# Kernel optimization log

Measured on AMD Instinct MI355X. Metric: run time of the kernel, lower is better.

The kernel has to match this reference:

```python
import jax, jax.numpy as jnp
import numpy as np

D = 128          # latent_dim
N = 40000        # num nodes
B = 8            # num graphs in batch
S = N // B       # nodes per graph
K = 6            # knn
E = 640000       # spatial edges
FF = 256         # ffn hidden


def glorot(key, shape):
    lim = jnp.sqrt(6.0 / (shape[0] + shape[-1]))
    return jax.random.uniform(key, shape, minval=-lim, maxval=lim, dtype=jnp.float32)


def setup_inputs() -> dict:
    key = jax.random.key(0)
    ks = jax.random.split(key, 24)
    inp = {
        "x": jax.random.normal(ks[0], (N, D), dtype=jnp.float32),
        "edge_index": jax.random.randint(ks[1], (2, E), 0, N, dtype=jnp.int64),
        "edge_attr": jax.random.uniform(ks[2], (E, 1), dtype=jnp.float32),
        "batch": jnp.repeat(jnp.arange(B, dtype=jnp.int64), S),
        # spatial GATv2Conv params
        "W_sl": glorot(ks[3], (D, D)), "b_sl": jnp.zeros((D,), jnp.float32),
        "W_sr": glorot(ks[4], (D, D)), "b_sr": jnp.zeros((D,), jnp.float32),
        "att_s": glorot(ks[5], (D,)), "W_se": glorot(ks[6], (1, D)),
        "bias_s": jnp.zeros((D,), jnp.float32),
        # latent GATv2Conv params (no edge features)
        "W_ll": glorot(ks[7], (D, D)), "b_ll": jnp.zeros((D,), jnp.float32),
        "W_lr": glorot(ks[8], (D, D)), "b_lr": jnp.zeros((D,), jnp.float32),
        "att_l": glorot(ks[9], (D,)), "bias_l": jnp.zeros((D,), jnp.float32),
        # concat_skip fusion linear: in = 2*D
        "W_c": glorot(ks[10], (2 * D, D)), "b_c": jnp.zeros((D,), jnp.float32),
        # FFN
        "W_f1": glorot(ks[11], (D, FF)), "b_f1": jnp.zeros((FF,), jnp.float32),
        "W_f2": glorot(ks[12], (FF, D)), "b_f2": jnp.zeros((D,), jnp.float32),
    }
    return inp


def relu6(v):
    return jnp.clip(v, 0.0, 6.0)


def segment_softmax(logits, seg, num_segments):
    m = jax.ops.segment_max(logits, seg, num_segments=num_segments)
    e = jnp.exp(logits - m[seg])
    s = jax.ops.segment_sum(e, seg, num_segments=num_segments)
    return e / s[seg]


def gatv2(x, src, dst, edge_feat, W_l, b_l, W_r, b_r, att, bias):
    """PyG GATv2Conv, heads=1, concat=True, negative_slope=0.2."""
    xl = x @ W_l + b_l            # [N,D] source transform
    xr = x @ W_r + b_r            # [N,D] target transform
    h = xl[src] + xr[dst]         # [E,D]
    if edge_feat is not None:
        h = h + edge_feat         # [E,D] already projected by lin_edge
    h = jax.nn.leaky_relu(h, 0.2)
    alpha = h @ att               # [E]
    alpha = segment_softmax(alpha, dst, N)
    out = jax.ops.segment_sum(xl[src] * alpha[:, None], dst, num_segments=N)
    return out + bias


def knn_edges(x):
    """knn_graph(k=K, loop=False, flow='source_to_target') per graph, plus
    the self loops that latent GATv2Conv adds (add_self_loops=True)."""
    xs = jax.lax.stop_gradient(x).reshape(B, S, D)
    sq = jnp.sum(xs * xs, axis=-1)                       # [B,S]
    d2 = sq[:, :, None] + sq[:, None, :] - 2.0 * jnp.einsum('bid,bjd->bij', xs, xs)
    d2 = jnp.where(jnp.eye(S, dtype=bool)[None], jnp.inf, d2)
    _, idx = jax.lax.top_k(-d2, K)                       # [B,S,K] neighbor ids
    offs = (jnp.arange(B) * S)[:, None, None]
    src = (idx + offs).reshape(-1)                       # neighbors -> sources
    dst = jnp.repeat(jnp.arange(N), K)                   # query nodes -> targets
    loop = jnp.arange(N)
    return jnp.concatenate([src, loop]), jnp.concatenate([dst, loop])


def reference(x, edge_index, edge_attr, batch,
              W_sl, b_sl, W_sr, b_sr, att_s, W_se, bias_s,
              W_ll, b_ll, W_lr, b_lr, att_l, bias_l,
              W_c, b_c, W_f1, b_f1, W_f2, b_f2):
    # spatial channel: GATv2 with scalar edge attr
    e_feat = edge_attr @ W_se                            # lin_edge, [E,D]
    ch_sp = gatv2(x, edge_index[0], edge_index[1], e_feat,
                  W_sl, b_sl, W_sr, b_sr, att_s, bias_s)
    # latent channel: dynamic kNN graph + GATv2
    src_l, dst_l = knn_edges(x)
    ch_lat = gatv2(x, src_l, dst_l, None,
                   W_ll, b_ll, W_lr, b_lr, att_l, bias_l)
    # fusion = concat_skip
    fused = jnp.concatenate([ch_sp, ch_lat], axis=-1) @ W_c + b_c + x
    # FFN block (norms are Identity), residual
    ffn = relu6(fused @ W_f1 + b_f1) @ W_f2 + b_f2
    out = fused + ffn
    # plain_last=False -> final activation relu6
    return relu6(out)
```

## Files before the change

### kernel.cpp

```cpp
#include <hip/hip_runtime.h>
#include <math.h>

constexpr int N  = 40000;
constexpr int D  = 128;
constexpr int E  = 640000;
constexpr int Bg = 8;
constexpr int Sg = 5000;
constexpr int KN = 6;
constexpr int FF = 256;
constexpr int QLEN = 1280;
constexpr int NCAND = 48;

typedef short short8 __attribute__((ext_vector_type(8)));
typedef float f32x4  __attribute__((ext_vector_type(4)));

__device__ __forceinline__ unsigned short f2bf(float f)
{
    unsigned int u = __float_as_uint(f);
    return (unsigned short)((u + 0x7fffu + ((u >> 16) & 1u)) >> 16);
}

__device__ __forceinline__ unsigned umin2(unsigned a, unsigned b) { return a < b ? a : b; }

__global__ __launch_bounds__(256) void w_prep_k(
    const float* __restrict__ W0, const float* __restrict__ W1,
    const float* __restrict__ W2, const float* __restrict__ W3,
    const float* __restrict__ Wc, const float* __restrict__ Wf1,
    const float* __restrict__ Wf2,
    unsigned short* __restrict__ wt4, unsigned short* __restrict__ wtc,
    unsigned short* __restrict__ wtf1, unsigned short* __restrict__ wtf2)
{
    int idx = blockIdx.x * 256 + threadIdx.x;
    if (idx < 65536) {
        int m = idx >> 14, rem = idx & 16383;
        int k = rem & 127, c = rem >> 7;
        const float* Wm = (m == 0) ? W0 : (m == 1) ? W1 : (m == 2) ? W2 : W3;
        wt4[m * 16384 + c * 128 + k] = f2bf(Wm[k * 128 + c]);
    } else if (idx < 98304) {
        int rem = idx - 65536; int k = rem & 255, c = rem >> 8;
        wtc[c * 256 + k] = f2bf(Wc[k * 128 + c]);
    } else if (idx < 131072) {
        int rem = idx - 98304; int k = rem & 127, c = rem >> 7;
        wtf1[c * 128 + k] = f2bf(Wf1[k * 256 + c]);
    } else {
        int rem = idx - 131072; int k = rem & 255, c = rem >> 8;
        wtf2[c * 256 + k] = f2bf(Wf2[k * 128 + c]);
    }
}

__global__ __launch_bounds__(256) void gemm_mfma_k(
    const float* __restrict__ A, int lda,
    const unsigned short* __restrict__ Wt, int Kdim,
    const float* __restrict__ bias,
    const float* __restrict__ res,
    float* __restrict__ out, int ldo, int act)
{
    __shared__ float xs[64][36];
    __shared__ unsigned short ws[128][40];
    int tid = threadIdx.x;
    int w = tid >> 6, lane = tid & 63;
    int lg = lane >> 4, ln = lane & 15;
    int r0 = blockIdx.x * 64;
    int cb = blockIdx.y * 128;

    f32x4 acc[8];
#pragma unroll
    for (int ct = 0; ct < 8; ++ct) acc[ct] = {0.f, 0.f, 0.f, 0.f};

    int srow = tid >> 2, sk8 = (tid & 3) * 8;
    int wcol = tid >> 1, wk = (tid & 1) * 16;

    for (int kt = 0; kt < Kdim; kt += 32) {
        __syncthreads();
        *(float4*)&xs[srow][sk8]     = *(const float4*)&A[(size_t)(r0 + srow) * lda + kt + sk8];
        *(float4*)&xs[srow][sk8 + 4] = *(const float4*)&A[(size_t)(r0 + srow) * lda + kt + sk8 + 4];
        *(short8*)&ws[wcol][wk]     = *(const short8*)&Wt[(size_t)(cb + wcol) * Kdim + kt + wk];
        *(short8*)&ws[wcol][wk + 8] = *(const short8*)&Wt[(size_t)(cb + wcol) * Kdim + kt + wk + 8];
        __syncthreads();

        int arow = w * 16 + ln;
        f32x4 a0 = *(const f32x4*)&xs[arow][lg * 8];
        f32x4 a1 = *(const f32x4*)&xs[arow][lg * 8 + 4];
        float af[8] = {a0[0], a0[1], a0[2], a0[3], a1[0], a1[1], a1[2], a1[3]};
        short8 ah, al;
#pragma unroll
        for (int i = 0; i < 8; ++i) {
            unsigned short h = f2bf(af[i]);
            ah[i] = (short)h;
            float hf = __uint_as_float(((unsigned)h) << 16);
            al[i] = (short)f2bf(af[i] - hf);
        }
#pragma unroll
        for (int ct = 0; ct < 8; ++ct) {
            short8 bw = *(const short8*)&ws[ct * 16 + ln][lg * 8];
            acc[ct] = __builtin_amdgcn_mfma_f32_16x16x32_bf16(ah, bw, acc[ct], 0, 0, 0);
            acc[ct] = __builtin_amdgcn_mfma_f32_16x16x32_bf16(al, bw, acc[ct], 0, 0, 0);
        }
    }

#pragma unroll
    for (int ct = 0; ct < 8; ++ct) {
        int c = cb + ct * 16 + ln;
        float bv = bias[c];
#pragma unroll
        for (int rg = 0; rg < 4; ++rg) {
            int r = r0 + w * 16 + lg * 4 + rg;
            float v = acc[ct][rg] + bv;
            if (res) v += res[(size_t)r * 128 + c];
            if (act) v = fminf(fmaxf(v, 0.f), 6.f);
            out[(size_t)r * ldo + c] = v;
        }
    }
}

__global__ __launch_bounds__(256) void gemm4_mfma_k(
    const float* __restrict__ A, const unsigned short* __restrict__ wt4,
    const float* __restrict__ b0, const float* __restrict__ b1,
    const float* __restrict__ b2, const float* __restrict__ b3,
    float* __restrict__ o0, float* __restrict__ o1,
    float* __restrict__ o2, float* __restrict__ o3)
{
    const unsigned short* Wt = wt4 + blockIdx.y * 16384;
    const float* bias; float* out;
    if (blockIdx.y == 0)      { bias = b0; out = o0; }
    else if (blockIdx.y == 1) { bias = b1; out = o1; }
    else if (blockIdx.y == 2) { bias = b2; out = o2; }
    else                      { bias = b3; out = o3; }

    __shared__ float xs[64][36];
    __shared__ unsigned short ws[128][40];
    int tid = threadIdx.x;
    int w = tid >> 6, lane = tid & 63;
    int lg = lane >> 4, ln = lane & 15;
    int r0 = blockIdx.x * 64;

    f32x4 acc[8];
#pragma unroll
    for (int ct = 0; ct < 8; ++ct) acc[ct] = {0.f, 0.f, 0.f, 0.f};

    int srow = tid >> 2, sk8 = (tid & 3) * 8;
    int wcol = tid >> 1, wk = (tid & 1) * 16;

    for (int kt = 0; kt < 128; kt += 32) {
        __syncthreads();
        *(float4*)&xs[srow][sk8]     = *(const float4*)&A[(size_t)(r0 + srow) * 128 + kt + sk8];
        *(float4*)&xs[srow][sk8 + 4] = *(const float4*)&A[(size_t)(r0 + srow) * 128 + kt + sk8 + 4];
        *(short8*)&ws[wcol][wk]     = *(const short8*)&Wt[(size_t)wcol * 128 + kt + wk];
        *(short8*)&ws[wcol][wk + 8] = *(const short8*)&Wt[(size_t)wcol * 128 + kt + wk + 8];
        __syncthreads();

        int arow = w * 16 + ln;
        f32x4 a0 = *(const f32x4*)&xs[arow][lg * 8];
        f32x4 a1 = *(const f32x4*)&xs[arow][lg * 8 + 4];
        float af[8] = {a0[0], a0[1], a0[2], a0[3], a1[0], a1[1], a1[2], a1[3]};
        short8 ah, al;
#pragma unroll
        for (int i = 0; i < 8; ++i) {
            unsigned short h = f2bf(af[i]);
            ah[i] = (short)h;
            float hf = __uint_as_float(((unsigned)h) << 16);
            al[i] = (short)f2bf(af[i] - hf);
        }
#pragma unroll
        for (int ct = 0; ct < 8; ++ct) {
            short8 bw = *(const short8*)&ws[ct * 16 + ln][lg * 8];
            acc[ct] = __builtin_amdgcn_mfma_f32_16x16x32_bf16(ah, bw, acc[ct], 0, 0, 0);
            acc[ct] = __builtin_amdgcn_mfma_f32_16x16x32_bf16(al, bw, acc[ct], 0, 0, 0);
        }
    }

#pragma unroll
    for (int ct = 0; ct < 8; ++ct) {
        int c = ct * 16 + ln;
        float bv = bias[c];
#pragma unroll
        for (int rg = 0; rg < 4; ++rg) {
            int r = r0 + w * 16 + lg * 4 + rg;
            out[(size_t)r * 128 + c] = acc[ct][rg] + bv;
        }
    }
}

__global__ __launch_bounds__(256) void prep_k(const float* __restrict__ x,
                                              unsigned short* __restrict__ xh,
                                              float* __restrict__ sqn)
{
    int w = threadIdx.x >> 6, lane = threadIdx.x & 63;
    int row = blockIdx.x * 4 + w;
    float2 v = *(const float2*)&x[(size_t)row * 128 + lane * 2];
    ushort2 h = make_ushort2(f2bf(v.x), f2bf(v.y));
    *(ushort2*)&xh[(size_t)row * 128 + lane * 2] = h;
    float s = fmaf(v.y, v.y, v.x * v.x);
#pragma unroll
    for (int off = 32; off; off >>= 1) s += __shfl_xor(s, off);
    if (lane == 0) sqn[row] = s;
}

__device__ __forceinline__ void ins6(unsigned (&d)[6], unsigned k)
{
#pragma unroll
    for (int t = 0; t < 6; ++t) {
        unsigned lo = d[t] < k ? d[t] : k;
        unsigned hi = d[t] < k ? k : d[t];
        d[t] = lo; k = hi;
    }
}

__global__ __launch_bounds__(256) void knn_mfma_k(const unsigned short* __restrict__ xh,
                                                  const float* __restrict__ sqn,
                                                  int* __restrict__ cand)
{
    __shared__ char lds[16640];
    char* ldsH = lds;
    float* cs_s = (float*)(lds + 16384);

    int b = blockIdx.x;
    int g = b & 7, r = b >> 3;
    int qtr = r & 3, qblk = r >> 2;
    int gbase = g * Sg;
    int cbase = qtr * QLEN;
    int qlen = (qtr < 3) ? QLEN : (Sg - 3 * QLEN);
    int ntiles = (qlen + 63) >> 6;
    int nfull = (qtr < 3) ? ntiles : ntiles - 1;
    int tid = threadIdx.x;
    int w = tid >> 6, lane = tid & 63;
    int lg = lane >> 4, ln = lane & 15;
    int q0 = qblk * 128 + w * 32;

    short8 bh[2][4];
#pragma unroll
    for (int s = 0; s < 2; ++s) {
        int q = q0 + s * 16 + ln;
        int qrow = gbase + (q < Sg ? q : Sg - 1);
#pragma unroll
        for (int ks = 0; ks < 4; ++ks)
            bh[s][ks] = *(const short8*)&xh[(size_t)qrow * 128 + ks * 32 + lg * 8];
    }

    int srow = tid >> 4, sslot = tid & 15;
    int sw_st = (srow & 7) << 4;
    int dstoff[4];
    const unsigned short* src[4];
#pragma unroll
    for (int i = 0; i < 4; ++i) {
        int row = i * 16 + srow;
        dstoff[i] = row * 256 + ((sslot * 16) ^ sw_st);
        src[i] = &xh[(size_t)(gbase + cbase + row) * 128 + sslot * 8];
    }
    const float* csrc = &sqn[gbase + cbase];

    unsigned d6a[6], d6b[6];
#pragma unroll
    for (int t = 0; t < 6; ++t) { d6a[t] = 0xFFFFFFFFu; d6b[t] = 0xFFFFFFFFu; }

    for (int t64 = 0; t64 < ntiles; ++t64) {
        __syncthreads();
        if (t64 < nfull) {
#pragma unroll
            for (int i = 0; i < 4; ++i) {
                short8 vh = *(const short8*)src[i];
                src[i] += 64 * 128;
                *(short8*)(ldsH + dstoff[i]) = vh;
            }
            if (tid < 64) cs_s[tid] = csrc[tid] + 1024.0f;
        } else {
            int c0 = cbase + t64 * 64;
#pragma unroll
            for (int i = 0; i < 4; ++i) {
                int cr = c0 + i * 16 + srow;
                if (cr >= Sg) cr = Sg - 1;
                short8 vh = *(const short8*)&xh[(size_t)(gbase + cr) * 128 + sslot * 8];
                *(short8*)(ldsH + dstoff[i]) = vh;
            }
            if (tid < 64) {
                int cl = c0 + tid;
                cs_s[tid] = (cl < cbase + qlen) ? (sqn[gbase + cl] + 1024.0f) : __builtin_inff();
            }
        }
        csrc += 64;
        __syncthreads();

        int c0 = cbase + t64 * 64;
#pragma unroll
        for (int g16 = 0; g16 < 4; ++g16) {
            f32x4 acc0 = {0.f, 0.f, 0.f, 0.f};
            f32x4 acc1 = {0.f, 0.f, 0.f, 0.f};
            int rr = g16 * 16 + ln;
            int rsw = (ln & 7) << 4;
#pragma unroll
            for (int ks = 0; ks < 4; ++ks) {
                short8 ah = *(const short8*)(ldsH + rr * 256 + ((lg * 16 + ks * 64) ^ rsw));
                acc0 = __builtin_amdgcn_mfma_f32_16x16x32_bf16(ah, bh[0][ks], acc0, 0, 0, 0);
                acc1 = __builtin_amdgcn_mfma_f32_16x16x32_bf16(ah, bh[1][ks], acc1, 0, 0, 0);
            }
            f32x4 cv = *(const f32x4*)&cs_s[g16 * 16 + lg * 4];
            int idx0 = (c0 - cbase) + g16 * 16 + lg * 4;
            unsigned kb0[4], kb1[4];
#pragma unroll
            for (int rg = 0; rg < 4; ++rg) {
                kb0[rg] = __float_as_uint(fmaf(-2.f, acc0[rg], cv[rg]));
                kb1[rg] = __float_as_uint(fmaf(-2.f, acc1[rg], cv[rg]));
            }
            unsigned mn0 = umin2(umin2(kb0[0], kb0[1]), umin2(kb0[2], kb0[3]));
            unsigned mn1 = umin2(umin2(kb1[0], kb1[1]), umin2(kb1[2], kb1[3]));
            if ((mn0 & 0xFFFFF800u) < d6a[5]) {
#pragma unroll
                for (int rg = 0; rg < 4; ++rg) {
                    unsigned k = (kb0[rg] & 0xFFFFF800u) | (unsigned)(idx0 + rg);
                    if (k < d6a[5]) ins6(d6a, k);
                }
            }
            if ((mn1 & 0xFFFFF800u) < d6b[5]) {
#pragma unroll
                for (int rg = 0; rg < 4; ++rg) {
                    unsigned k = (kb1[rg] & 0xFFFFF800u) | (unsigned)(idx0 + rg);
                    if (k < d6b[5]) ins6(d6b, k);
                }
            }
        }
    }

#pragma unroll
    for (int s = 0; s < 2; ++s) {
        unsigned m12[12];
#pragma unroll
        for (int t = 0; t < 6; ++t) m12[t] = s ? d6b[t] : d6a[t];
#pragma unroll
        for (int t = 6; t < 12; ++t) m12[t] = 0xFFFFFFFFu;
#pragma unroll
        for (int sg = 1; sg < 4; ++sg)
#pragma unroll
            for (int t = 0; t < 6; ++t) {
                unsigned v = __shfl(s ? d6b[t] : d6a[t], ln + sg * 16);
#pragma unroll
                for (int u = 0; u < 12; ++u) {
                    unsigned lo = m12[u] < v ? m12[u] : v;
                    unsigned hi = m12[u] < v ? v : m12[u];
                    m12[u] = lo; v = hi;
                }
            }
        int q = q0 + s * 16 + ln;
        if (lg == 0 && q < Sg) {
            int* cp = &cand[(size_t)(gbase + q) * NCAND + qtr * 12];
#pragma unroll
            for (int t = 0; t < 12; ++t) cp[t] = gbase + cbase + (int)(m12[t] & 2047u);
        }
    }
}

__global__ __launch_bounds__(256) void knn_rerank_k(const float* __restrict__ x,
                                                    const float* __restrict__ sqn,
                                                    const int* __restrict__ cand,
                                                    int* __restrict__ knn_idx)
{
    int w = threadIdx.x >> 6, lane = threadIdx.x & 63;
    int grp = lane >> 4, gl = lane & 15;
    int q = blockIdx.x * 4 + w;
    float4 qa = *(const float4*)&x[(size_t)q * 128 + gl * 8];
    float4 qb = *(const float4*)&x[(size_t)q * 128 + gl * 8 + 4];
    const int* cp = &cand[(size_t)q * NCAND + grp * 12];

    float d6[6]; int i6[6]; float mx = __builtin_inff(); int sl = 0;
#pragma unroll
    for (int t = 0; t < 6; ++t) { d6[t] = __builtin_inff(); i6[t] = -1; }

#pragma unroll 2
    for (int j = 0; j < 12; ++j) {
        int c = cp[j];
        bool ok = (unsigned)c < (unsigned)N && c != q;
        int ca = ok ? c : 0;
        float4 va = *(const float4*)&x[(size_t)ca * 128 + gl * 8];
        float4 vb = *(const float4*)&x[(size_t)ca * 128 + gl * 8 + 4];
        float p = qa.x * va.x;
        p = fmaf(qa.y, va.y, p); p = fmaf(qa.z, va.z, p); p = fmaf(qa.w, va.w, p);
        p = fmaf(qb.x, vb.x, p); p = fmaf(qb.y, vb.y, p);
        p = fmaf(qb.z, vb.z, p); p = fmaf(qb.w, vb.w, p);
#pragma unroll
        for (int off = 1; off < 16; off <<= 1) p += __shfl_xor(p, off);
        float dv = ok ? fmaf(-2.f, p, sqn[ca]) : __builtin_inff();
        if (dv < mx) {
#pragma unroll
            for (int t = 0; t < 6; ++t)
                if (t == sl) { d6[t] = dv; i6[t] = c; }
            float m2 = d6[0]; int s2 = 0;
#pragma unroll
            for (int t = 1; t < 6; ++t)
                if (d6[t] > m2) { m2 = d6[t]; s2 = t; }
            mx = m2; sl = s2;
        }
    }

#pragma unroll
    for (int sg = 1; sg < 4; ++sg) {
#pragma unroll
        for (int t = 0; t < 6; ++t) {
            float dv = __shfl(d6[t], gl + sg * 16);
            int ci = __shfl(i6[t], gl + sg * 16);
            if (grp == 0 && dv < mx) {
#pragma unroll
                for (int u = 0; u < 6; ++u)
                    if (u == sl) { d6[u] = dv; i6[u] = ci; }
                float m2 = d6[0]; int s2 = 0;
#pragma unroll
                for (int u = 1; u < 6; ++u)
                    if (d6[u] > m2) { m2 = d6[u]; s2 = u; }
                mx = m2; sl = s2;
            }
        }
    }
    if (lane < 6) {
        int v;
#pragma unroll
        for (int t = 0; t < 6; ++t) if (t == lane) v = i6[t];
        knn_idx[(size_t)q * 6 + lane] = v;
    }
}

__global__ __launch_bounds__(256) void hist_k(const int* __restrict__ dstA, int* __restrict__ deg)
{
    int e = blockIdx.x * 256 + threadIdx.x;
    atomicAdd(&deg[dstA[e]], 1);
}

__global__ __launch_bounds__(1024) void scan_k(const int* __restrict__ deg, int* __restrict__ rowptr)
{
    __shared__ int ps[1024];
    int t = threadIdx.x;
    const int chunk = 40;
    int base = t * chunk;
    int s = 0;
    for (int k = 0; k < chunk; ++k) { int i = base + k; if (i < N) s += deg[i]; }
    ps[t] = s;
    __syncthreads();
    for (int off = 1; off < 1024; off <<= 1) {
        int v = (t >= off) ? ps[t - off] : 0;
        __syncthreads();
        ps[t] += v;
        __syncthreads();
    }
    int run = ps[t] - s;
    for (int k = 0; k < chunk; ++k) {
        int i = base + k;
        if (i < N) { rowptr[i] = run; run += deg[i]; }
    }
    if (t == 0) rowptr[N] = E;
}

__global__ __launch_bounds__(256) void scatter_k(const int* __restrict__ srcA, const int* __restrict__ dstA,
                                                 const float* __restrict__ ea,
                                                 const int* __restrict__ rowptr, int* __restrict__ cnt,
                                                 int* __restrict__ csr_src, float* __restrict__ csr_ea)
{
    int e = blockIdx.x * 256 + threadIdx.x;
    int d = dstA[e];
    int pos = rowptr[d] + atomicAdd(&cnt[d], 1);
    csr_src[pos] = srcA[e];
    csr_ea[pos] = ea[e];
}

__global__ __launch_bounds__(256) void gat_fused_k(
    const float* __restrict__ xl_s, const float* __restrict__ xr_s,
    const int* __restrict__ rowptr, const int* __restrict__ csr_src, const float* __restrict__ csr_ea,
    const float* __restrict__ att_s, const float* __restrict__ wse, const float* __restrict__ bias_s,
    const float* __restrict__ xl_l, const float* __restrict__ xr_l,
    const int* __restrict__ knn, const float* __restrict__ att_l, const float* __restrict__ bias_l,
    float* __restrict__ ch2)
{
    int w = threadIdx.x >> 6, lane = threadIdx.x & 63;
    int dst = blockIdx.x * 4 + w;

    if (blockIdx.y == 0) {
        int base = rowptr[dst];
        int deg = rowptr[dst + 1] - base;
        float xr0 = xr_s[(size_t)dst * 128 + lane], xr1 = xr_s[(size_t)dst * 128 + 64 + lane];
        float at0 = att_s[lane], at1 = att_s[64 + lane];
        float we0 = wse[lane], we1 = wse[64 + lane];

        float m = -1e30f, ssum = 0.f, o0 = 0.f, o1 = 0.f;
        for (int i = 0; i < deg; ++i) {
            int s = csr_src[base + i];
            float ea = csr_ea[base + i];
            float v0 = xl_s[(size_t)s * 128 + lane];
            float v1 = xl_s[(size_t)s * 128 + 64 + lane];
            float h0 = fmaf(ea, we0, v0 + xr0);
            float h1 = fmaf(ea, we1, v1 + xr1);
            h0 = h0 > 0.f ? h0 : 0.2f * h0;
            h1 = h1 > 0.f ? h1 : 0.2f * h1;
            float p = fmaf(h1, at1, h0 * at0);
#pragma unroll
            for (int off = 32; off; off >>= 1) p += __shfl_xor(p, off);
            if (p <= m) {
                float wt = __expf(p - m);
                ssum += wt;
                o0 = fmaf(wt, v0, o0);
                o1 = fmaf(wt, v1, o1);
            } else {
                float sc = __expf(m - p);
                ssum = fmaf(ssum, sc, 1.f);
                o0 = fmaf(o0, sc, v0);
                o1 = fmaf(o1, sc, v1);
                m = p;
            }
        }
        float inv = deg > 0 ? 1.f / ssum : 0.f;
        ch2[(size_t)dst * 256 + lane]      = fmaf(o0, inv, bias_s[lane]);
        ch2[(size_t)dst * 256 + 64 + lane] = fmaf(o1, inv, bias_s[64 + lane]);
    } else {
        float xr0 = xr_l[(size_t)dst * 128 + lane], xr1 = xr_l[(size_t)dst * 128 + 64 + lane];
        float at0 = att_l[lane], at1 = att_l[64 + lane];
        int s[7];
#pragma unroll
        for (int j = 0; j < 6; ++j) s[j] = knn[(size_t)dst * 6 + j];
        s[6] = dst;
        float l[7];
#pragma unroll
        for (int j = 0; j < 7; ++j) {
            float h0 = xl_l[(size_t)s[j] * 128 + lane] + xr0;
            float h1 = xl_l[(size_t)s[j] * 128 + 64 + lane] + xr1;
            h0 = h0 > 0.f ? h0 : 0.2f * h0;
            h1 = h1 > 0.f ? h1 : 0.2f * h1;
            float p = h0 * at0 + h1 * at1;
#pragma unroll
            for (int off = 32; off; off >>= 1) p += __shfl_xor(p, off);
            l[j] = p;
        }
        float m = l[0];
#pragma unroll
        for (int j = 1; j < 7; ++j) m = fmaxf(m, l[j]);
        float sum = 0.f;
#pragma unroll
        for (int j = 0; j < 7; ++j) { l[j] = __expf(l[j] - m); sum += l[j]; }
        float inv = 1.f / sum;
        float o0 = 0.f, o1 = 0.f;
#pragma unroll
        for (int j = 0; j < 7; ++j) {
            float a = l[j] * inv;
            o0 = fmaf(a, xl_l[(size_t)s[j] * 128 + lane], o0);
            o1 = fmaf(a, xl_l[(size_t)s[j] * 128 + 64 + lane], o1);
        }
        ch2[(size_t)dst * 256 + 128 + lane] = o0 + bias_l[lane];
        ch2[(size_t)dst * 256 + 192 + lane] = o1 + bias_l[64 + lane];
    }
}

extern "C" void kernel_launch(void* const* d_in, const int* in_sizes, int n_in,
                              void* d_out, int out_size, void* d_ws, size_t ws_size,
                              hipStream_t stream)
{
    const float* x      = (const float*)d_in[0];
    const int*   ei     = (const int*)  d_in[1];
    const float* eattr  = (const float*)d_in[2];
    const float* W_sl   = (const float*)d_in[4];
    const float* b_sl   = (const float*)d_in[5];
    const float* W_sr   = (const float*)d_in[6];
    const float* b_sr   = (const float*)d_in[7];
    const float* att_s  = (const float*)d_in[8];
    const float* W_se   = (const float*)d_in[9];
    const float* bias_s = (const float*)d_in[10];
    const float* W_ll   = (const float*)d_in[11];
    const float* b_ll   = (const float*)d_in[12];
    const float* W_lr   = (const float*)d_in[13];
    const float* b_lr   = (const float*)d_in[14];
    const float* att_l  = (const float*)d_in[15];
    const float* bias_l = (const float*)d_in[16];
    const float* W_c    = (const float*)d_in[17];
    const float* b_c    = (const float*)d_in[18];
    const float* W_f1   = (const float*)d_in[19];
    const float* b_f1   = (const float*)d_in[20];
    const float* W_f2   = (const float*)d_in[21];
    const float* b_f2   = (const float*)d_in[22];
    float* out = (float*)d_out;

    char* wp = (char*)d_ws;
    auto take = [&](size_t bytes) { char* p = wp; wp += (bytes + 255) & ~(size_t)255; return p; };
    float* xl_s    = (float*)take((size_t)N * D * 4);
    float* xr_s    = (float*)take((size_t)N * D * 4);
    float* xl_l    = (float*)take((size_t)N * D * 4);
    float* xr_l    = (float*)take((size_t)N * D * 4);
    float* ch2     = (float*)take((size_t)N * 2 * D * 4);
    float* sqn     = (float*)take((size_t)N * 4);
    int*   knn_idx = (int*)  take((size_t)N * KN * 4);
    int*   deg     = (int*)  take((size_t)N * 4);
    int*   rowptr  = (int*)  take((size_t)(N + 1) * 4);
    int*   csr_src = (int*)  take((size_t)E * 4);
    float* csr_ea  = (float*)take((size_t)E * 4);
    unsigned short* x_hi = (unsigned short*)take((size_t)N * D * 2);
    int*   knn_cand = (int*)take((size_t)N * NCAND * 4);
    unsigned short* wt4  = (unsigned short*)take(65536 * 2);
    unsigned short* wtc  = (unsigned short*)take(32768 * 2);
    unsigned short* wtf1 = (unsigned short*)take(32768 * 2);
    unsigned short* wtf2 = (unsigned short*)take(32768 * 2);
    float* fused   = xl_s;
    float* hbuf    = ch2;
    if ((size_t)(wp - (char*)d_ws) > ws_size) return;

    dim3 blk(256);

    w_prep_k<<<dim3(640), blk, 0, stream>>>(W_sl, W_sr, W_ll, W_lr, W_c, W_f1, W_f2,
                                            wt4, wtc, wtf1, wtf2);

    gemm4_mfma_k<<<dim3(N / 64, 4), blk, 0, stream>>>(x, wt4,
        b_sl, b_sr, b_ll, b_lr, xl_s, xr_s, xl_l, xr_l);

    prep_k<<<dim3(N / 4), blk, 0, stream>>>(x, x_hi, sqn);
    knn_mfma_k<<<dim3(Bg * 40 * 4), blk, 0, stream>>>(x_hi, sqn, knn_cand);
    knn_rerank_k<<<dim3(N / 4), blk, 0, stream>>>(x, sqn, knn_cand, knn_idx);

    hipMemsetAsync(deg, 0, (size_t)N * 4, stream);
    hist_k<<<dim3(E / 256), blk, 0, stream>>>(ei + E, deg);
    scan_k<<<dim3(1), dim3(1024), 0, stream>>>(deg, rowptr);
    hipMemsetAsync(deg, 0, (size_t)N * 4, stream);
    scatter_k<<<dim3(E / 256), blk, 0, stream>>>(ei, ei + E, eattr, rowptr, deg, csr_src, csr_ea);

    gat_fused_k<<<dim3(N / 4, 2), blk, 0, stream>>>(xl_s, xr_s, rowptr, csr_src, csr_ea,
                                                    att_s, W_se, bias_s,
                                                    xl_l, xr_l, knn_idx, att_l, bias_l, ch2);

    gemm_mfma_k<<<dim3(N / 64, 1), blk, 0, stream>>>(ch2, 2 * D, wtc, 256, b_c, x, fused, 128, 0);
    gemm_mfma_k<<<dim3(N / 64, 2), blk, 0, stream>>>(fused, 128, wtf1, 128, b_f1, nullptr, hbuf, 256, 1);
    gemm_mfma_k<<<dim3(N / 64, 1), blk, 0, stream>>>(hbuf, 256, wtf2, 256, b_f2, fused, out, 128, 1);
}
```

Before: 570.6 us.

## Split kNN candidate scan into eighths, prefetch gathers in rerank and GAT loops

```diff
diff --git a/kernel.cpp b/kernel.cpp
--- a/kernel.cpp
+++ b/kernel.cpp
@@ -8,7 +8,7 @@
 constexpr int Sg = 5000;
 constexpr int KN = 6;
 constexpr int FF = 256;
-constexpr int QLEN = 1280;
+constexpr int CLEN = 640;
 constexpr int NCAND = 48;
 
 typedef short short8 __attribute__((ext_vector_type(8)));
@@ -19,8 +19,6 @@
     unsigned int u = __float_as_uint(f);
     return (unsigned short)((u + 0x7fffu + ((u >> 16) & 1u)) >> 16);
 }
-
-__device__ __forceinline__ unsigned umin2(unsigned a, unsigned b) { return a < b ? a : b; }
 
 __global__ __launch_bounds__(256) void w_prep_k(
     const float* __restrict__ W0, const float* __restrict__ W1,
@@ -216,12 +214,12 @@
 
     int b = blockIdx.x;
     int g = b & 7, r = b >> 3;
-    int qtr = r & 3, qblk = r >> 2;
+    int chunk = r & 7, qblk = r >> 3;
     int gbase = g * Sg;
-    int cbase = qtr * QLEN;
-    int qlen = (qtr < 3) ? QLEN : (Sg - 3 * QLEN);
+    int cbase = chunk * CLEN;
+    int qlen = (chunk < 7) ? CLEN : (Sg - 7 * CLEN);
     int ntiles = (qlen + 63) >> 6;
-    int nfull = (qtr < 3) ? ntiles : ntiles - 1;
+    int nfull = (chunk < 7) ? ntiles : ntiles - 1;
     int tid = threadIdx.x;
     int w = tid >> 6, lane = tid & 63;
     int lg = lane >> 4, ln = lane & 15;
@@ -295,55 +293,39 @@
             }
             f32x4 cv = *(const f32x4*)&cs_s[g16 * 16 + lg * 4];
             int idx0 = (c0 - cbase) + g16 * 16 + lg * 4;
-            unsigned kb0[4], kb1[4];
 #pragma unroll
             for (int rg = 0; rg < 4; ++rg) {
-                kb0[rg] = __float_as_uint(fmaf(-2.f, acc0[rg], cv[rg]));
-                kb1[rg] = __float_as_uint(fmaf(-2.f, acc1[rg], cv[rg]));
-            }
-            unsigned mn0 = umin2(umin2(kb0[0], kb0[1]), umin2(kb0[2], kb0[3]));
-            unsigned mn1 = umin2(umin2(kb1[0], kb1[1]), umin2(kb1[2], kb1[3]));
-            if ((mn0 & 0xFFFFF800u) < d6a[5]) {
-#pragma unroll
-                for (int rg = 0; rg < 4; ++rg) {
-                    unsigned k = (kb0[rg] & 0xFFFFF800u) | (unsigned)(idx0 + rg);
-                    if (k < d6a[5]) ins6(d6a, k);
-                }
-            }
-            if ((mn1 & 0xFFFFF800u) < d6b[5]) {
-#pragma unroll
-                for (int rg = 0; rg < 4; ++rg) {
-                    unsigned k = (kb1[rg] & 0xFFFFF800u) | (unsigned)(idx0 + rg);
-                    if (k < d6b[5]) ins6(d6b, k);
-                }
+                unsigned ki = (unsigned)(idx0 + rg);
+                unsigned k0 = (__float_as_uint(fmaf(-2.f, acc0[rg], cv[rg])) & 0xFFFFF800u) | ki;
+                unsigned k1 = (__float_as_uint(fmaf(-2.f, acc1[rg], cv[rg])) & 0xFFFFF800u) | ki;
+                ins6(d6a, k0);
+                ins6(d6b, k1);
             }
         }
     }
 
 #pragma unroll
     for (int s = 0; s < 2; ++s) {
-        unsigned m12[12];
-#pragma unroll
-        for (int t = 0; t < 6; ++t) m12[t] = s ? d6b[t] : d6a[t];
-#pragma unroll
-        for (int t = 6; t < 12; ++t) m12[t] = 0xFFFFFFFFu;
+        unsigned m6[6];
+#pragma unroll
+        for (int t = 0; t < 6; ++t) m6[t] = s ? d6b[t] : d6a[t];
 #pragma unroll
         for (int sg = 1; sg < 4; ++sg)
 #pragma unroll
             for (int t = 0; t < 6; ++t) {
                 unsigned v = __shfl(s ? d6b[t] : d6a[t], ln + sg * 16);
 #pragma unroll
-                for (int u = 0; u < 12; ++u) {
-                    unsigned lo = m12[u] < v ? m12[u] : v;
-                    unsigned hi = m12[u] < v ? v : m12[u];
-                    m12[u] = lo; v = hi;
+                for (int u = 0; u < 6; ++u) {
+                    unsigned lo = m6[u] < v ? m6[u] : v;
+                    unsigned hi = m6[u] < v ? v : m6[u];
+                    m6[u] = lo; v = hi;
                 }
             }
         int q = q0 + s * 16 + ln;
         if (lg == 0 && q < Sg) {
-            int* cp = &cand[(size_t)(gbase + q) * NCAND + qtr * 12];
-#pragma unroll
-            for (int t = 0; t < 12; ++t) cp[t] = gbase + cbase + (int)(m12[t] & 2047u);
+            int* cp = &cand[(size_t)(gbase + q) * NCAND + chunk * 6];
+#pragma unroll
+            for (int t = 0; t < 6; ++t) cp[t] = gbase + cbase + (int)(m6[t] & 2047u);
         }
     }
 }
@@ -360,34 +342,46 @@
     float4 qb = *(const float4*)&x[(size_t)q * 128 + gl * 8 + 4];
     const int* cp = &cand[(size_t)q * NCAND + grp * 12];
 
-    float d6[6]; int i6[6]; float mx = __builtin_inff(); int sl = 0;
-#pragma unroll
-    for (int t = 0; t < 6; ++t) { d6[t] = __builtin_inff(); i6[t] = -1; }
-
-#pragma unroll 2
+    int ca[12]; unsigned okm = 0;
+#pragma unroll
     for (int j = 0; j < 12; ++j) {
         int c = cp[j];
         bool ok = (unsigned)c < (unsigned)N && c != q;
-        int ca = ok ? c : 0;
-        float4 va = *(const float4*)&x[(size_t)ca * 128 + gl * 8];
-        float4 vb = *(const float4*)&x[(size_t)ca * 128 + gl * 8 + 4];
-        float p = qa.x * va.x;
-        p = fmaf(qa.y, va.y, p); p = fmaf(qa.z, va.z, p); p = fmaf(qa.w, va.w, p);
-        p = fmaf(qb.x, vb.x, p); p = fmaf(qb.y, vb.y, p);
-        p = fmaf(qb.z, vb.z, p); p = fmaf(qb.w, vb.w, p);
+        okm |= (ok ? 1u : 0u) << j;
+        ca[j] = ok ? c : 0;
+    }
+
+    float d6[6]; int i6[6]; float mx = __builtin_inff(); int sl = 0;
+#pragma unroll
+    for (int t = 0; t < 6; ++t) { d6[t] = __builtin_inff(); i6[t] = -1; }
+
+    float4 vaA = *(const float4*)&x[(size_t)ca[0] * 128 + gl * 8];
+    float4 vbA = *(const float4*)&x[(size_t)ca[0] * 128 + gl * 8 + 4];
+#pragma unroll
+    for (int j = 0; j < 12; ++j) {
+        float4 vaB, vbB;
+        if (j < 11) {
+            vaB = *(const float4*)&x[(size_t)ca[j + 1] * 128 + gl * 8];
+            vbB = *(const float4*)&x[(size_t)ca[j + 1] * 128 + gl * 8 + 4];
+        }
+        float p = qa.x * vaA.x;
+        p = fmaf(qa.y, vaA.y, p); p = fmaf(qa.z, vaA.z, p); p = fmaf(qa.w, vaA.w, p);
+        p = fmaf(qb.x, vbA.x, p); p = fmaf(qb.y, vbA.y, p);
+        p = fmaf(qb.z, vbA.z, p); p = fmaf(qb.w, vbA.w, p);
 #pragma unroll
         for (int off = 1; off < 16; off <<= 1) p += __shfl_xor(p, off);
-        float dv = ok ? fmaf(-2.f, p, sqn[ca]) : __builtin_inff();
+        float dv = ((okm >> j) & 1u) ? fmaf(-2.f, p, sqn[ca[j]]) : __builtin_inff();
         if (dv < mx) {
 #pragma unroll
             for (int t = 0; t < 6; ++t)
-                if (t == sl) { d6[t] = dv; i6[t] = c; }
+                if (t == sl) { d6[t] = dv; i6[t] = ca[j]; }
             float m2 = d6[0]; int s2 = 0;
 #pragma unroll
             for (int t = 1; t < 6; ++t)
                 if (d6[t] > m2) { m2 = d6[t]; s2 = t; }
             mx = m2; sl = s2;
         }
+        vaA = vaB; vbA = vbB;
     }
 
 #pragma unroll
@@ -476,12 +470,22 @@
         float at0 = att_s[lane], at1 = att_s[64 + lane];
         float we0 = wse[lane], we1 = wse[64 + lane];
 
+        float eaN = 0.f, v0N = 0.f, v1N = 0.f;
+        if (deg > 0) {
+            int s0 = csr_src[base];
+            eaN = csr_ea[base];
+            v0N = xl_s[(size_t)s0 * 128 + lane];
+            v1N = xl_s[(size_t)s0 * 128 + 64 + lane];
+        }
         float m = -1e30f, ssum = 0.f, o0 = 0.f, o1 = 0.f;
         for (int i = 0; i < deg; ++i) {
-            int s = csr_src[base + i];
-            float ea = csr_ea[base + i];
-            float v0 = xl_s[(size_t)s * 128 + lane];
-            float v1 = xl_s[(size_t)s * 128 + 64 + lane];
+            float ea = eaN, v0 = v0N, v1 = v1N;
+            if (i + 1 < deg) {
+                int sn = csr_src[base + i + 1];
+                eaN = csr_ea[base + i + 1];
+                v0N = xl_s[(size_t)sn * 128 + lane];
+                v1N = xl_s[(size_t)sn * 128 + 64 + lane];
+            }
             float h0 = fmaf(ea, we0, v0 + xr0);
             float h1 = fmaf(ea, we1, v1 + xr1);
             h0 = h0 > 0.f ? h0 : 0.2f * h0;
@@ -603,7 +607,7 @@
         b_sl, b_sr, b_ll, b_lr, xl_s, xr_s, xl_l, xr_l);
 
     prep_k<<<dim3(N / 4), blk, 0, stream>>>(x, x_hi, sqn);
-    knn_mfma_k<<<dim3(Bg * 40 * 4), blk, 0, stream>>>(x_hi, sqn, knn_cand);
+    knn_mfma_k<<<dim3(Bg * 40 * 8), blk, 0, stream>>>(x_hi, sqn, knn_cand);
     knn_rerank_k<<<dim3(N / 4), blk, 0, stream>>>(x, sqn, knn_cand, knn_idx);
 
     hipMemsetAsync(deg, 0, (size_t)N * 4, stream);
```

After: 521.2 us. 8.7% less time.
